# Performance work log

Hardware: AMD Instinct MI355X
Metric: run time of the kernel (lower is better)

## Reference

```python
import jax, jax.numpy as jnp
import numpy as np
from jax import lax

B, CIN, HID, COUT = 64, 256, 256, 10
MULTI, KS = 3, 3
TH = TW = 7      # template (kernel) input spatial size
SH = SW = 31     # search input spatial size
EPS = 1e-5
DN = ('NCHW', 'OIHW', 'NCHW')


def _conv(x, w):
    return lax.conv_general_dilated(x, w, (1, 1), 'VALID', dimension_numbers=DN)


def _bn(x, p):
    # p: [4, C] packed (gamma, beta, running_mean, running_var); inference-mode BN
    g, b, m, v = p[0], p[1], p[2], p[3]
    inv = g / jnp.sqrt(v + EPS)
    return x * inv[:, None, None] + (b - m * inv)[:, None, None]


def _dwxcorr(x, k):
    # per-sample depthwise cross-correlation via groups = B*C trick
    b, c, h, w = x.shape
    kh, kw = k.shape[2], k.shape[3]
    y = lax.conv_general_dilated(
        x.reshape(1, b * c, h, w), k.reshape(b * c, 1, kh, kw),
        (1, 1), 'VALID', dimension_numbers=DN, feature_group_count=b * c)
    return y.reshape(b, c, y.shape[2], y.shape[3])


def _multixcorr(search, kernel):
    # crop template feature to 5x5 / 3x3 / 1x1 sub-kernels, xcorr each,
    # center-crop outputs to the common (smallest) size, concat on channels
    kh = kernel.shape[2]
    feats = []
    for i in range(MULTI):
        kk = kernel[:, :, i:kh - i, i:kh - i]
        o = _dwxcorr(search, kk)
        if i > 0:
            o = o[:, :, i:o.shape[2] - i, i:o.shape[3] - i]
        feats.append(o)
    return jnp.concatenate(feats, axis=1)  # [B, MULTI*HID, 25, 25]


def setup_inputs() -> dict:
    key = jax.random.key(0)
    ks = jax.random.split(key, 12)
    f32 = jnp.float32
    return {
        'kernel': jax.random.normal(ks[0], (B, CIN, TH, TW), f32),
        'search': jax.random.normal(ks[1], (B, CIN, SH, SW), f32),
        'wk': jax.random.normal(ks[2], (HID, CIN, KS, KS), f32) * 0.05,
        'bnk': jax.random.uniform(ks[3], (4, HID), f32, 0.1, 1.0),
        'ws': jax.random.normal(ks[4], (HID, CIN, KS, KS), f32) * 0.05,
        'bns': jax.random.uniform(ks[5], (4, HID), f32, 0.1, 1.0),
        'wd': jax.random.normal(ks[6], (HID, CIN * MULTI, 1, 1), f32) * 0.05,
        'bnd': jax.random.uniform(ks[7], (4, HID), f32, 0.1, 1.0),
        'wh1': jax.random.normal(ks[8], (HID, HID, 1, 1), f32) * 0.05,
        'bnh': jax.random.uniform(ks[9], (4, HID), f32, 0.1, 1.0),
        'wh2': jax.random.normal(ks[10], (COUT, HID, 1, 1), f32) * 0.05,
        'bh2': jax.random.normal(ks[11], (COUT,), f32) * 0.05,
    }


def reference(kernel, search, wk, bnk, ws, bns, wd, bnd, wh1, bnh, wh2, bh2):
    k = jax.nn.relu(_bn(_conv(kernel, wk), bnk))   # [B, HID, 5, 5]
    s = jax.nn.relu(_bn(_conv(search, ws), bns))   # [B, HID, 29, 29]
    feature = _multixcorr(s, k)                    # [B, 3*HID, 25, 25]
    feature = _bn(_conv(feature, wd), bnd)         # [B, HID, 25, 25]
    h = jax.nn.relu(_bn(_conv(feature, wh1), bnh))
    out = _conv(h, wh2) + bh2[:, None, None]       # [B, COUT, 25, 25]
    return out
```

## Files before the change

kernel.cpp:

```cpp
#include <hip/hip_runtime.h>
#include <hip/hip_bf16.h>
#include <cstdint>
#include <cstddef>

#define EPSBN 1e-5f

typedef unsigned short u16;
typedef unsigned int u32;
typedef _Float16 f16;
typedef _Float16 f16x8 __attribute__((ext_vector_type(8)));
typedef float f32x4 __attribute__((ext_vector_type(4)));

__device__ __forceinline__ void async_copy16(void* lds, const void* g) {
    __builtin_amdgcn_global_load_lds(
        (const __attribute__((address_space(1))) u32*)g,
        (__attribute__((address_space(3))) u32*)lds, 16, 0, 0);
}

__global__ __launch_bounds__(256) void prep_all(
    const float* __restrict__ sin, f16* __restrict__ sa,
    const float* __restrict__ kin, f16* __restrict__ ka,
    const float* __restrict__ wk, const float* __restrict__ ws,
    const float* __restrict__ wd, const float* __restrict__ wh1,
    const float* __restrict__ wh2, f16* __restrict__ bpk,
    f16* __restrict__ bps, f16* __restrict__ bpd, f16* __restrict__ bp1,
    f16* __restrict__ bp2) {
    __shared__ float tile[64][65];
    int t = blockIdx.x;
    int tid = threadIdx.x;
    if (t < 4352) {
        int b = t / 68;
        int rem = t - b * 68;
        int c0 = (rem / 17) * 64;
        int z = rem % 17;
        bool isk = (z == 16);
        const float* in = isk ? kin : sin;
        f16* op = isk ? ka : sa;
        int HW = isk ? 49 : 961;
        int h0 = isk ? 0 : z * 64;
        int cl = tid >> 6;
        int hl = tid & 63;
        for (int r = cl; r < 64; r += 4) {
            int hw = h0 + hl;
            tile[r][hl] =
                (hw < HW) ? in[(size_t)(b * 256 + c0 + r) * HW + hw] : 0.f;
        }
        __syncthreads();
        int c = tid & 63;
        for (int r = cl; r < 64; r += 4) {
            int hw = h0 + r;
            if (hw < HW)
                op[((size_t)b * HW + hw) * 256 + c0 + c] = (f16)tile[c][r];
        }
        return;
    }
    int blk = t - 4352;
    const float* W;
    f16* Bp;
    int nK32, OCr, K, i;
    bool conv = false;
    if (blk < 2304) {
        W = wk; Bp = bpk; nK32 = 72; OCr = 256; K = 2304; conv = true;
        i = blk * 256 + tid;
    } else if (blk < 4608) {
        W = ws; Bp = bps; nK32 = 72; OCr = 256; K = 2304; conv = true;
        i = (blk - 2304) * 256 + tid;
    } else if (blk < 5376) {
        W = wd; Bp = bpd; nK32 = 24; OCr = 256; K = 768;
        i = (blk - 4608) * 256 + tid;
    } else if (blk < 5632) {
        W = wh1; Bp = bp1; nK32 = 8; OCr = 256; K = 256;
        i = (blk - 5376) * 256 + tid;
    } else {
        W = wh2; Bp = bp2; nK32 = 8; OCr = 10; K = 256;
        i = (blk - 5632) * 256 + tid;
    }
    int per = nK32 * 512;
    int oct = i / per;
    int r = i - oct * per;
    int k32 = r >> 9;
    int lr = r & 511;
    int l = lr >> 3, j = lr & 7;
    int oc = oct * 16 + (l & 15);
    int k = k32 * 32 + ((l >> 4) << 3) + j;
    float v = 0.f;
    if (oc < OCr)
        v = conv ? W[(size_t)(oc * 256 + (k & 255)) * 9 + (k >> 8)]
                 : W[(size_t)oc * K + k];
    Bp[(size_t)(oct * nK32 + k32) * 512 + lr] = (f16)v;
}

template <int KHW, int EPI>
__device__ __forceinline__ void gemm8_body(
    f16* lds, const f16* __restrict__ A, const f16* __restrict__ Bp,
    const float* __restrict__ bnp, float* __restrict__ outF,
    f16* __restrict__ oF, int m0, int M, int OC, int C, int H, int W,
    int OH, int OW) {
    const int Ktot = KHW * C;
    const int nKt = Ktot >> 6;
    const int nI = nKt >> 1;
    const int nK32 = Ktot >> 5;
    const int tid = threadIdx.x;
    const int lane = tid & 63;
    const int wid = tid >> 6;
    const int rowl = lane & 15;
    const int quad = lane >> 4;
    const int wm = wid >> 2;
    const int wn = wid & 3;
    const int OHW = OH * OW;

    int arow[4];
#pragma unroll
    for (int h = 0; h < 2; ++h)
#pragma unroll
        for (int s = 0; s < 2; ++s) {
            int ml = ((wid & 4) << 5) + h * 64 + (wid & 3) * 16 + s * 8 +
                     (lane >> 3);
            int m = m0 + ml;
            if (m >= M) m = M - 1;
            int b = m / OHW;
            int r = m - b * OHW;
            int y = r / OW;
            int x = r - y * OW;
            arow[h * 2 + s] = ((b * H + y) * W + x) * C +
                              (((lane & 7) ^ (lane >> 3)) << 3);
        }
    int bsrcb[2];
#pragma unroll
    for (int h = 0; h < 2; ++h) {
        int slot = h * 8 + wid;
        int o = ((slot >> 1) & 3) * 4 + ((slot >> 3) << 1) + (slot & 1);
        bsrcb[h] = o * nK32 * 512 + lane * 8;
    }

    auto koff_of = [&](int kt) {
        if (KHW == 9) {
            int pos = kt >> 2;
            int ky = pos / 3, kx = pos - ky * 3;
            return (ky * W + kx) * C + ((kt & 3) << 6);
        }
        return kt << 6;
    };
    auto stageA = [&](int buf, int h, int kt) {
        int koff = koff_of(kt);
#pragma unroll
        for (int s = 0; s < 2; ++s)
            async_copy16(
                &lds[buf * 16384 +
                     ((h * 1024 + wid * 128 + s * 64 + lane) << 3)],
                A + arow[h * 2 + s] + koff);
    };
    auto stageB = [&](int buf, int h, int kt) {
#pragma unroll
        for (int s = 0; s < 2; ++s)
            async_copy16(
                &lds[32768 + buf * 16384 +
                     ((((h * 8 + wid) * 2 + s) * 64 + lane) << 3)],
                Bp + bsrcb[h] + (kt * 2 + s) * 512);
    };

    f32x4 acc[8][4];
#pragma unroll
    for (int i = 0; i < 8; ++i)
#pragma unroll
        for (int j = 0; j < 4; ++j) acc[i][j] = (f32x4)0.f;

    f16x8 ah[4][2], bhA[2][2], bhB[2][2];

    auto dsA = [&](int buf, int qm) {
#pragma unroll
        for (int ii = 0; ii < 4; ++ii) {
            int g = qm * 128 + wm * 64 + ii * 16 + rowl;
#pragma unroll
            for (int ks = 0; ks < 2; ++ks)
                ah[ii][ks] = *(const f16x8*)&lds[
                    buf * 16384 + g * 64 +
                    ((((ks << 2) | quad) ^ (rowl & 7)) << 3)];
        }
    };
    auto dsB = [&](int buf, int qn, f16x8 (&bh)[2][2]) {
#pragma unroll
        for (int jj = 0; jj < 2; ++jj) {
            int slot = qn * 8 + wn * 2 + jj;
#pragma unroll
            for (int ks = 0; ks < 2; ++ks)
                bh[jj][ks] = *(const f16x8*)&lds[
                    32768 + buf * 16384 + (slot * 2 + ks) * 512 + lane * 8];
        }
    };

#define MFMA_QUAD(qm, qn, bh)                                            \
    do {                                                                 \
        _Pragma("unroll") for (int ks = 0; ks < 2; ++ks)                 \
            _Pragma("unroll") for (int ii = 0; ii < 4; ++ii)             \
                _Pragma("unroll") for (int jj = 0; jj < 2; ++jj)         \
                    acc[(qm)*4 + ii][(qn)*2 + jj] =                      \
                        __builtin_amdgcn_mfma_f32_16x16x32_f16(          \
                            ah[ii][ks], bh[jj][ks],                      \
                            acc[(qm)*4 + ii][(qn)*2 + jj], 0, 0, 0);     \
    } while (0)

#define PH_TAIL(MF)                                        \
    __builtin_amdgcn_s_barrier();                          \
    asm volatile("s_waitcnt lgkmcnt(0)" ::: "memory");     \
    __builtin_amdgcn_s_setprio(1);                         \
    MF;                                                    \
    __builtin_amdgcn_s_setprio(0)

    stageA(0, 0, 0);
    stageA(0, 1, 0);
    stageB(0, 0, 0);
    stageB(0, 1, 0);
    stageA(1, 0, 1);
    stageB(1, 0, 1);
    stageB(1, 1, 1);
    asm volatile("s_waitcnt vmcnt(6)" ::: "memory");
    __builtin_amdgcn_s_barrier();

    for (int it = 0; it < nI; ++it) {
        const bool more = (it + 1 < nI);
        const int t2 = 2 * it + 2;
        const int t3 = 2 * it + 3;
        dsA(0, 0);
        dsB(0, 0, bhA);
        stageA(1, 1, 2 * it + 1);
        PH_TAIL(MFMA_QUAD(0, 0, bhA));
        __builtin_amdgcn_s_barrier();
        dsB(0, 1, bhB);
        if (more) stageA(0, 0, t2);
        PH_TAIL(MFMA_QUAD(0, 1, bhB));
        __builtin_amdgcn_s_barrier();
        dsA(0, 1);
        if (more) stageB(0, 0, t2);
        PH_TAIL(MFMA_QUAD(1, 0, bhA));
        __builtin_amdgcn_s_barrier();
        if (more) stageB(0, 1, t2);
        PH_TAIL(MFMA_QUAD(1, 1, bhB));
        if (more)
            asm volatile("s_waitcnt vmcnt(6)" ::: "memory");
        else
            asm volatile("s_waitcnt vmcnt(0)" ::: "memory");
        __builtin_amdgcn_s_barrier();
        dsA(1, 0);
        dsB(1, 0, bhA);
        if (more) stageA(0, 1, t2);
        PH_TAIL(MFMA_QUAD(0, 0, bhA));
        __builtin_amdgcn_s_barrier();
        dsB(1, 1, bhB);
        if (more) stageA(1, 0, t3);
        PH_TAIL(MFMA_QUAD(0, 1, bhB));
        __builtin_amdgcn_s_barrier();
        dsA(1, 1);
        if (more) stageB(1, 0, t3);
        PH_TAIL(MFMA_QUAD(1, 0, bhA));
        __builtin_amdgcn_s_barrier();
        if (more) stageB(1, 1, t3);
        PH_TAIL(MFMA_QUAD(1, 1, bhB));
        if (more) asm volatile("s_waitcnt vmcnt(6)" ::: "memory");
        __builtin_amdgcn_s_barrier();
    }
#undef PH_TAIL
#undef MFMA_QUAD

#pragma unroll
    for (int j = 0; j < 4; ++j) {
        int oc = wn * 64 + j * 16 + rowl;
        bool ocv = oc < OC;
        float scale = 1.f, shift = 0.f;
        if (ocv) {
            if (EPI != 3) {
                float g = bnp[oc];
                float bb = bnp[OC + oc];
                float mm = bnp[2 * OC + oc];
                float vv = bnp[3 * OC + oc];
                float inv = g * rsqrtf(vv + EPSBN);
                scale = inv;
                shift = bb - mm * inv;
            } else {
                shift = bnp[oc];
            }
        }
#pragma unroll
        for (int i = 0; i < 8; ++i) {
#pragma unroll
            for (int r = 0; r < 4; ++r) {
                int m = m0 + wm * 128 + i * 16 + quad * 4 + r;
                if (m < M && ocv) {
                    float v = acc[i][j][r] * scale + shift;
                    if (EPI == 2) v = fmaxf(v, 0.f);
                    if (EPI == 3) {
                        int b = m / OHW;
                        int rr = m - b * OHW;
                        outF[((size_t)b * OC + oc) * OHW + rr] = v;
                    } else {
                        oF[(size_t)m * OC + oc] = (f16)v;
                    }
                }
            }
        }
    }
}

__global__ __launch_bounds__(512, 2) void conv33_fused8(
    const f16* sA_g, const f16* bpS, const float* bns, f16* sOut,
    const f16* kA_g, const f16* bpK, const float* bnk, f16* kOut) {
    __shared__ f16 lds[65536];
    bool sec = blockIdx.x < 7;
    const f16* A = sec ? kA_g : sA_g;
    const f16* Bp = sec ? bpK : bpS;
    const float* bnp = sec ? bnk : bns;
    f16* oF = sec ? kOut : sOut;
    int M = sec ? 1600 : 53824;
    int Hh = sec ? 7 : 31;
    int OHs = sec ? 5 : 29;
    int m0 = (sec ? blockIdx.x : (blockIdx.x - 7)) * 256;
    gemm8_body<9, 2>(lds, A, Bp, bnp, nullptr, oF, m0, M, 256, 256, Hh, Hh,
                     OHs, OHs);
}

__global__ __launch_bounds__(256, 2) void head_fused(
    const f16* __restrict__ feat, const f16* __restrict__ bpd,
    const float* __restrict__ bnd, const f16* __restrict__ bp1,
    const float* __restrict__ bnh, const f16* __restrict__ bp2,
    const float* __restrict__ bh2, float* __restrict__ out) {
    __shared__ f16 lds[40960];
    const int F2B = 20480;
    const int tid = threadIdx.x;
    const int lane = tid & 63;
    const int rowl = lane & 15;
    const int quad = lane >> 4;
    const int wn = tid >> 6;
    const int m0 = blockIdx.x * 80;

    int asrc[5];
#pragma unroll
    for (int s = 0; s < 5; ++s) {
        int idx = tid + s * 256;
        int ml = idx >> 4;
        int qs = (idx & 15) ^ (ml & 15);
        asrc[s] = ml * 768 + qs * 8;
    }
    auto issueA = [&](int buf, int kb) {
#pragma unroll
        for (int s = 0; s < 5; ++s)
            async_copy16(&lds[buf * 10240 + (tid + s * 256) * 8],
                         feat + (size_t)m0 * 768 + asrc[s] + kb * 128);
    };
    auto loadB = [&](f16x8(&bh)[4][4], const f16* __restrict__ Bp, int nK32,
                     int kb) {
#pragma unroll
        for (int ks = 0; ks < 4; ++ks)
#pragma unroll
            for (int j = 0; j < 4; ++j)
                bh[ks][j] = *(const f16x8*)&Bp[((size_t)((wn * 4 + j) * nK32 +
                                                         kb * 4 + ks)) *
                                                   512 +
                                               lane * 8];
    };

    f32x4 acc[5][4];
#pragma unroll
    for (int i = 0; i < 5; ++i)
#pragma unroll
        for (int j = 0; j < 4; ++j) acc[i][j] = (f32x4)0.f;

    auto computeS1 = [&](int buf, f16x8(&bh)[4][4]) {
#pragma unroll
        for (int ks = 0; ks < 4; ++ks) {
            f16x8 ah[5];
#pragma unroll
            for (int i = 0; i < 5; ++i)
                ah[i] = *(const f16x8*)&lds[buf * 10240 +
                                            (i * 16 + rowl) * 128 +
                                            ((((ks << 2) | quad) ^ rowl)
                                             << 3)];
#pragma unroll
            for (int i = 0; i < 5; ++i)
#pragma unroll
                for (int j = 0; j < 4; ++j)
                    acc[i][j] = __builtin_amdgcn_mfma_f32_16x16x32_f16(
                        ah[i], bh[ks][j], acc[i][j], 0, 0, 0);
        }
    };
    auto tileRd = [&](int kb, int ks, int i) {
        int g = i * 16 + rowl;
        int kc = kb * 16 + (ks << 2) + quad;
        int sw = (kc & 24) | ((kc ^ rowl) & 7);
        return *(const f16x8*)&lds[F2B + g * 256 + (sw << 3)];
    };

    f16x8 bh0[4][4], bh1[4][4];
    issueA(0, 0);
    loadB(bh0, bpd, 24, 0);
    for (int kb = 0; kb < 6; kb += 2) {
        __syncthreads();
        issueA(1, kb + 1);
        loadB(bh1, bpd, 24, kb + 1);
        computeS1(0, bh0);
        __syncthreads();
        if (kb + 2 < 6) {
            issueA(0, kb + 2);
            loadB(bh0, bpd, 24, kb + 2);
        }
        computeS1(1, bh1);
    }
#pragma unroll
    for (int j = 0; j < 4; ++j) {
        int oc = wn * 64 + j * 16 + rowl;
        float g = bnd[oc], bb = bnd[256 + oc], mm = bnd[512 + oc],
              vv = bnd[768 + oc];
        float inv = g * rsqrtf(vv + EPSBN);
        float shift = bb - mm * inv;
        int c = oc >> 3;
#pragma unroll
        for (int i = 0; i < 5; ++i)
#pragma unroll
            for (int r = 0; r < 4; ++r) {
                int row = i * 16 + quad * 4 + r;
                int sw = (c & 24) | ((c ^ row) & 7);
                lds[F2B + row * 256 + (sw << 3) + (oc & 7)] =
                    (f16)(acc[i][j][r] * inv + shift);
            }
    }
    loadB(bh0, bp1, 8, 0);
    __syncthreads();

#pragma unroll
    for (int i = 0; i < 5; ++i)
#pragma unroll
        for (int j = 0; j < 4; ++j) acc[i][j] = (f32x4)0.f;
    loadB(bh1, bp1, 8, 1);
#pragma unroll
    for (int kb = 0; kb < 2; ++kb) {
#pragma unroll
        for (int ks = 0; ks < 4; ++ks) {
            f16x8 ah[5];
#pragma unroll
            for (int i = 0; i < 5; ++i) ah[i] = tileRd(kb, ks, i);
#pragma unroll
            for (int i = 0; i < 5; ++i)
#pragma unroll
                for (int j = 0; j < 4; ++j)
                    acc[i][j] = __builtin_amdgcn_mfma_f32_16x16x32_f16(
                        ah[i], kb ? bh1[ks][j] : bh0[ks][j], acc[i][j], 0, 0,
                        0);
        }
    }
    __syncthreads();
#pragma unroll
    for (int j = 0; j < 4; ++j) {
        int oc = wn * 64 + j * 16 + rowl;
        float g = bnh[oc], bb = bnh[256 + oc], mm = bnh[512 + oc],
              vv = bnh[768 + oc];
        float inv = g * rsqrtf(vv + EPSBN);
        float shift = bb - mm * inv;
        int c = oc >> 3;
#pragma unroll
        for (int i = 0; i < 5; ++i)
#pragma unroll
            for (int r = 0; r < 4; ++r) {
                int row = i * 16 + quad * 4 + r;
                int sw = (c & 24) | ((c ^ row) & 7);
                lds[F2B + row * 256 + (sw << 3) + (oc & 7)] =
                    (f16)fmaxf(acc[i][j][r] * inv + shift, 0.f);
            }
    }
    __syncthreads();
    if (wn != 0) return;

    f32x4 a3[5];
#pragma unroll
    for (int i = 0; i < 5; ++i) a3[i] = (f32x4)0.f;
#pragma unroll
    for (int kb = 0; kb < 2; ++kb)
#pragma unroll
        for (int ks = 0; ks < 4; ++ks) {
            f16x8 b3 =
                *(const f16x8*)&bp2[(size_t)(kb * 4 + ks) * 512 + lane * 8];
#pragma unroll
            for (int i = 0; i < 5; ++i)
                a3[i] = __builtin_amdgcn_mfma_f32_16x16x32_f16(
                    tileRd(kb, ks, i), b3, a3[i], 0, 0, 0);
        }
    int oc = rowl;
    if (oc < 10) {
        float shift = bh2[oc];
#pragma unroll
        for (int i = 0; i < 5; ++i)
#pragma unroll
            for (int r = 0; r < 4; ++r) {
                int m = m0 + i * 16 + quad * 4 + r;
                int b = m / 625;
                int rr = m - b * 625;
                out[((size_t)b * 10 + oc) * 625 + rr] = a3[i][r] + shift;
            }
    }
}

__global__ __launch_bounds__(256) void xcorr_nhwc(
    const f16* __restrict__ sf, const f16* __restrict__ kf,
    f16* __restrict__ feat) {
    int by = blockIdx.x;
    int b = by / 25;
    int y = by - b * 25;
    int c = threadIdx.x;
    float kv[25];
#pragma unroll
    for (int p = 0; p < 25; ++p)
        kv[p] = (float)kf[(size_t)(b * 25 + p) * 256 + c];
    const f16* srow = sf + (size_t)(b * 29 + y) * 29 * 256 + c;
    float sv[25];
#pragma unroll
    for (int d = 0; d < 5; ++d)
#pragma unroll
        for (int e = 0; e < 5; ++e)
            sv[d * 5 + e] = (float)srow[(size_t)(d * 29 + e) * 256];
#pragma unroll
    for (int x = 0; x < 25; ++x) {
        float a2 = sv[12] * kv[12];
        float a1 = a2;
#pragma unroll
        for (int d = 1; d < 4; ++d)
#pragma unroll
            for (int e = 1; e < 4; ++e)
                if (d != 2 || e != 2)
                    a1 = fmaf(sv[d * 5 + e], kv[d * 5 + e], a1);
        float a0 = a1;
#pragma unroll
        for (int p = 0; p < 25; ++p) {
            int d = p / 5, e = p % 5;
            if (d == 0 || d == 4 || e == 0 || e == 4)
                a0 = fmaf(sv[p], kv[p], a0);
        }
        size_t o = ((size_t)by * 25 + x) * 768 + c;
        feat[o] = (f16)a0;
        feat[o + 256] = (f16)a1;
        feat[o + 512] = (f16)a2;
        if (x < 24) {
#pragma unroll
            for (int d = 0; d < 5; ++d) {
#pragma unroll
                for (int e = 0; e < 4; ++e) sv[d * 5 + e] = sv[d * 5 + e + 1];
                sv[d * 5 + 4] = (float)srow[(size_t)(d * 29 + x + 5) * 256];
            }
        }
    }
}

extern "C" void kernel_launch(void* const* d_in, const int* in_sizes, int n_in,
                              void* d_out, int out_size, void* d_ws,
                              size_t ws_size, hipStream_t stream) {
    const float* kernel_in = (const float*)d_in[0];
    const float* search_in = (const float*)d_in[1];
    const float* wk = (const float*)d_in[2];
    const float* bnk = (const float*)d_in[3];
    const float* ws = (const float*)d_in[4];
    const float* bns = (const float*)d_in[5];
    const float* wd = (const float*)d_in[6];
    const float* bnd = (const float*)d_in[7];
    const float* wh1 = (const float*)d_in[8];
    const float* bnh = (const float*)d_in[9];
    const float* wh2 = (const float*)d_in[10];
    const float* bh2 = (const float*)d_in[11];
    float* out = (float*)d_out;

    char* base = (char*)d_ws;
    size_t off = 0;
    auto alloc = [&](size_t bytes) {
        off = (off + 511) & ~(size_t)511;
        void* p = base + off;
        off += bytes;
        return p;
    };

    f16* bpd = (f16*)alloc((size_t)16 * 24 * 512 * 2);
    f16* bp1 = (f16*)alloc((size_t)16 * 8 * 512 * 2);
    f16* bp2 = (f16*)alloc((size_t)8 * 8 * 512 * 2);
    f16* kfeat = (f16*)alloc((size_t)1600 * 256 * 2);
    f16* sfeat = (f16*)alloc((size_t)53824 * 256 * 2);
    size_t P1 = (off + 511) & ~(size_t)511;
    f16* bpk = (f16*)alloc((size_t)16 * 72 * 512 * 2);
    f16* bps = (f16*)alloc((size_t)16 * 72 * 512 * 2);
    f16* ka = (f16*)alloc((size_t)64 * 49 * 256 * 2);
    f16* sa = (f16*)alloc((size_t)64 * 961 * 256 * 2);
    f16* feat = (f16*)(base + P1);

    prep_all<<<dim3(10112), 256, 0, stream>>>(search_in, sa, kernel_in, ka,
                                              wk, ws, wd, wh1, wh2, bpk, bps,
                                              bpd, bp1, bp2);
    conv33_fused8<<<dim3(218), 512, 0, stream>>>(sa, bps, bns, sfeat, ka,
                                                 bpk, bnk, kfeat);
    xcorr_nhwc<<<dim3(1600), 256, 0, stream>>>(sfeat, kfeat, feat);
    head_fused<<<dim3(500), 256, 0, stream>>>(feat, bpd, bnd, bp1, bnh, bp2,
                                              bh2, out);
}
```

Measured before the change: 269.2 us.

## Fuse depthwise xcorr into head kernel, computing features directly into LDS

```diff
diff --git a/kernel.cpp b/kernel.cpp
--- a/kernel.cpp
+++ b/kernel.cpp
@@ -8,6 +8,8 @@
 typedef unsigned short u16;
 typedef unsigned int u32;
 typedef _Float16 f16;
+typedef _Float16 f16x2 __attribute__((ext_vector_type(2)));
+typedef _Float16 f16x4 __attribute__((ext_vector_type(4)));
 typedef _Float16 f16x8 __attribute__((ext_vector_type(8)));
 typedef float f32x4 __attribute__((ext_vector_type(4)));
 
@@ -15,6 +17,24 @@
     __builtin_amdgcn_global_load_lds(
         (const __attribute__((address_space(1))) u32*)g,
         (__attribute__((address_space(3))) u32*)lds, 16, 0, 0);
+}
+
+template <int NK32, int OCR, int KK, bool CONV>
+__device__ __forceinline__ void pack_w(const float* __restrict__ W,
+                                       f16* __restrict__ Bp, int i) {
+    const int per = NK32 * 512;
+    int oct = i / per;
+    int r = i - oct * per;
+    int k32 = r >> 9;
+    int lr = r & 511;
+    int l = lr >> 3, j = lr & 7;
+    int oc = oct * 16 + (l & 15);
+    int k = k32 * 32 + ((l >> 4) << 3) + j;
+    float v = 0.f;
+    if (oc < OCR)
+        v = CONV ? W[(size_t)(oc * 256 + (k & 255)) * 9 + (k >> 8)]
+                 : W[(size_t)oc * KK + k];
+    Bp[(size_t)(oct * NK32 + k32) * 512 + lr] = (f16)v;
 }
 
 __global__ __launch_bounds__(256) void prep_all(
@@ -46,48 +66,31 @@
                 (hw < HW) ? in[(size_t)(b * 256 + c0 + r) * HW + hw] : 0.f;
         }
         __syncthreads();
-        int c = tid & 63;
-        for (int r = cl; r < 64; r += 4) {
+        int cg = (tid & 15) * 4;
+        int rw = tid >> 4;
+#pragma unroll
+        for (int it = 0; it < 4; ++it) {
+            int r = rw + it * 16;
             int hw = h0 + r;
-            if (hw < HW)
-                op[((size_t)b * HW + hw) * 256 + c0 + c] = (f16)tile[c][r];
+            if (hw < HW) {
+                f16x4 v = {(f16)tile[cg][r], (f16)tile[cg + 1][r],
+                           (f16)tile[cg + 2][r], (f16)tile[cg + 3][r]};
+                *(f16x4*)&op[((size_t)b * HW + hw) * 256 + c0 + cg] = v;
+            }
         }
         return;
     }
     int blk = t - 4352;
-    const float* W;
-    f16* Bp;
-    int nK32, OCr, K, i;
-    bool conv = false;
-    if (blk < 2304) {
-        W = wk; Bp = bpk; nK32 = 72; OCr = 256; K = 2304; conv = true;
-        i = blk * 256 + tid;
-    } else if (blk < 4608) {
-        W = ws; Bp = bps; nK32 = 72; OCr = 256; K = 2304; conv = true;
-        i = (blk - 2304) * 256 + tid;
-    } else if (blk < 5376) {
-        W = wd; Bp = bpd; nK32 = 24; OCr = 256; K = 768;
-        i = (blk - 4608) * 256 + tid;
-    } else if (blk < 5632) {
-        W = wh1; Bp = bp1; nK32 = 8; OCr = 256; K = 256;
-        i = (blk - 5376) * 256 + tid;
-    } else {
-        W = wh2; Bp = bp2; nK32 = 8; OCr = 10; K = 256;
-        i = (blk - 5632) * 256 + tid;
-    }
-    int per = nK32 * 512;
-    int oct = i / per;
-    int r = i - oct * per;
-    int k32 = r >> 9;
-    int lr = r & 511;
-    int l = lr >> 3, j = lr & 7;
-    int oc = oct * 16 + (l & 15);
-    int k = k32 * 32 + ((l >> 4) << 3) + j;
-    float v = 0.f;
-    if (oc < OCr)
-        v = conv ? W[(size_t)(oc * 256 + (k & 255)) * 9 + (k >> 8)]
-                 : W[(size_t)oc * K + k];
-    Bp[(size_t)(oct * nK32 + k32) * 512 + lr] = (f16)v;
+    if (blk < 2304)
+        pack_w<72, 256, 2304, true>(wk, bpk, blk * 256 + tid);
+    else if (blk < 4608)
+        pack_w<72, 256, 2304, true>(ws, bps, (blk - 2304) * 256 + tid);
+    else if (blk < 5376)
+        pack_w<24, 256, 768, false>(wd, bpd, (blk - 4608) * 256 + tid);
+    else if (blk < 5632)
+        pack_w<8, 256, 256, false>(wh1, bp1, (blk - 5376) * 256 + tid);
+    else
+        pack_w<8, 10, 256, false>(wh2, bp2, (blk - 5632) * 256 + tid);
 }
 
 template <int KHW, int EPI>
@@ -319,10 +322,11 @@
 }
 
 __global__ __launch_bounds__(256, 2) void head_fused(
-    const f16* __restrict__ feat, const f16* __restrict__ bpd,
-    const float* __restrict__ bnd, const f16* __restrict__ bp1,
-    const float* __restrict__ bnh, const f16* __restrict__ bp2,
-    const float* __restrict__ bh2, float* __restrict__ out) {
+    const f16* __restrict__ sf, const f16* __restrict__ kf,
+    const f16* __restrict__ bpd, const float* __restrict__ bnd,
+    const f16* __restrict__ bp1, const float* __restrict__ bnh,
+    const f16* __restrict__ bp2, const float* __restrict__ bh2,
+    float* __restrict__ out) {
     __shared__ f16 lds[40960];
     const int F2B = 20480;
     const int tid = threadIdx.x;
@@ -331,21 +335,10 @@
     const int quad = lane >> 4;
     const int wn = tid >> 6;
     const int m0 = blockIdx.x * 80;
-
-    int asrc[5];
-#pragma unroll
-    for (int s = 0; s < 5; ++s) {
-        int idx = tid + s * 256;
-        int ml = idx >> 4;
-        int qs = (idx & 15) ^ (ml & 15);
-        asrc[s] = ml * 768 + qs * 8;
-    }
-    auto issueA = [&](int buf, int kb) {
-#pragma unroll
-        for (int s = 0; s < 5; ++s)
-            async_copy16(&lds[buf * 10240 + (tid + s * 256) * 8],
-                         feat + (size_t)m0 * 768 + asrc[s] + kb * 128);
-    };
+    const int c = tid;
+    const int cx = c >> 3;
+    const int c7 = c & 7;
+
     auto loadB = [&](f16x8(&bh)[4][4], const f16* __restrict__ Bp, int nK32,
                      int kb) {
 #pragma unroll
@@ -357,6 +350,12 @@
                                                    512 +
                                                lane * 8];
     };
+    auto tileRdAt = [&](int base, int w, int ks, int i) {
+        int g = i * 16 + rowl;
+        int kc = w * 16 + (ks << 2) + quad;
+        int sw = (kc & 24) | ((kc ^ rowl) & 7);
+        return *(const f16x8*)&lds[base + g * 256 + (sw << 3)];
+    };
 
     f32x4 acc[5][4];
 #pragma unroll
@@ -364,16 +363,12 @@
 #pragma unroll
         for (int j = 0; j < 4; ++j) acc[i][j] = (f32x4)0.f;
 
-    auto computeS1 = [&](int buf, f16x8(&bh)[4][4]) {
+    auto computeW = [&](int base, int w, f16x8(&bh)[4][4]) {
 #pragma unroll
         for (int ks = 0; ks < 4; ++ks) {
             f16x8 ah[5];
 #pragma unroll
-            for (int i = 0; i < 5; ++i)
-                ah[i] = *(const f16x8*)&lds[buf * 10240 +
-                                            (i * 16 + rowl) * 128 +
-                                            ((((ks << 2) | quad) ^ rowl)
-                                             << 3)];
+            for (int i = 0; i < 5; ++i) ah[i] = tileRdAt(base, w, ks, i);
 #pragma unroll
             for (int i = 0; i < 5; ++i)
 #pragma unroll
@@ -382,28 +377,102 @@
                         ah[i], bh[ks][j], acc[i][j], 0, 0, 0);
         }
     };
-    auto tileRd = [&](int kb, int ks, int i) {
-        int g = i * 16 + rowl;
-        int kc = kb * 16 + (ks << 2) + quad;
-        int sw = (kc & 24) | ((kc ^ rowl) & 7);
-        return *(const f16x8*)&lds[F2B + g * 256 + (sw << 3)];
-    };
-
+
+    {
+        int row = 0;
+        while (row < 80) {
+            int m = m0 + row;
+            int b = m / 625;
+            int rem = m - b * 625;
+            int y = rem / 25;
+            int x0 = rem - y * 25;
+            int len = 25 - x0;
+            if (len > 80 - row) len = 80 - row;
+            float kv[25];
+#pragma unroll
+            for (int p = 0; p < 25; ++p)
+                kv[p] = (float)kf[(size_t)(b * 25 + p) * 256 + c];
+            const f16* srow =
+                sf + ((size_t)(b * 29 + y) * 29 + x0) * 256 + c;
+            float sv[25];
+#pragma unroll
+            for (int d = 0; d < 5; ++d)
+#pragma unroll
+                for (int e = 0; e < 5; ++e)
+                    sv[d * 5 + e] = (float)srow[(size_t)(d * 29 + e) * 256];
+            for (int xx = 0;; ++xx) {
+                float a1 = 0.f;
+#pragma unroll
+                for (int d = 1; d < 4; ++d)
+#pragma unroll
+                    for (int e = 1; e < 4; ++e)
+                        a1 = fmaf(sv[d * 5 + e], kv[d * 5 + e], a1);
+                float a0 = a1;
+#pragma unroll
+                for (int p = 0; p < 25; ++p) {
+                    int d = p / 5, e = p % 5;
+                    if (d == 0 || d == 4 || e == 0 || e == 4)
+                        a0 = fmaf(sv[p], kv[p], a0);
+                }
+                int r = row + xx;
+                int swz = ((cx & 24) | ((cx ^ r) & 7)) << 3;
+                lds[r * 256 + swz + c7] = (f16)a0;
+                lds[F2B + r * 256 + swz + c7] = (f16)a1;
+                if (xx + 1 >= len) break;
+#pragma unroll
+                for (int d = 0; d < 5; ++d) {
+#pragma unroll
+                    for (int e = 0; e < 4; ++e)
+                        sv[d * 5 + e] = sv[d * 5 + e + 1];
+                    sv[d * 5 + 4] =
+                        (float)srow[(size_t)(d * 29 + xx + 5) * 256];
+                }
+            }
+            row += len;
+        }
+    }
     f16x8 bh0[4][4], bh1[4][4];
-    issueA(0, 0);
     loadB(bh0, bpd, 24, 0);
-    for (int kb = 0; kb < 6; kb += 2) {
-        __syncthreads();
-        issueA(1, kb + 1);
-        loadB(bh1, bpd, 24, kb + 1);
-        computeS1(0, bh0);
-        __syncthreads();
-        if (kb + 2 < 6) {
-            issueA(0, kb + 2);
-            loadB(bh0, bpd, 24, kb + 2);
-        }
-        computeS1(1, bh1);
-    }
+    __syncthreads();
+
+    loadB(bh1, bpd, 24, 1);
+    computeW(0, 0, bh0);
+    loadB(bh0, bpd, 24, 2);
+    computeW(0, 1, bh1);
+    __syncthreads();
+
+    {
+        int row = 0;
+        while (row < 80) {
+            int m = m0 + row;
+            int b = m / 625;
+            int rem = m - b * 625;
+            int y = rem / 25;
+            int x0 = rem - y * 25;
+            int len = 25 - x0;
+            if (len > 80 - row) len = 80 - row;
+            float k12 = (float)kf[(size_t)(b * 25 + 12) * 256 + c];
+            const f16* sp =
+                sf + ((size_t)(b * 29 + y + 2) * 29 + x0 + 2) * 256 + c;
+            for (int xx = 0; xx < len; ++xx) {
+                float a = (float)sp[(size_t)xx * 256] * k12;
+                int r = row + xx;
+                int swz = ((cx & 24) | ((cx ^ r) & 7)) << 3;
+                lds[r * 256 + swz + c7] = (f16)a;
+            }
+            row += len;
+        }
+    }
+    loadB(bh1, bpd, 24, 3);
+    computeW(F2B, 0, bh0);
+    computeW(F2B, 1, bh1);
+    loadB(bh0, bpd, 24, 4);
+    loadB(bh1, bpd, 24, 5);
+    __syncthreads();
+
+    computeW(0, 0, bh0);
+    computeW(0, 1, bh1);
+
 #pragma unroll
     for (int j = 0; j < 4; ++j) {
         int oc = wn * 64 + j * 16 + rowl;
@@ -411,13 +480,13 @@
               vv = bnd[768 + oc];
         float inv = g * rsqrtf(vv + EPSBN);
         float shift = bb - mm * inv;
-        int c = oc >> 3;
+        int cc = oc >> 3;
 #pragma unroll
         for (int i = 0; i < 5; ++i)
 #pragma unroll
             for (int r = 0; r < 4; ++r) {
                 int row = i * 16 + quad * 4 + r;
-                int sw = (c & 24) | ((c ^ row) & 7);
+                int sw = (cc & 24) | ((cc ^ row) & 7);
                 lds[F2B + row * 256 + (sw << 3) + (oc & 7)] =
                     (f16)(acc[i][j][r] * inv + shift);
             }
@@ -430,22 +499,8 @@
 #pragma unroll
         for (int j = 0; j < 4; ++j) acc[i][j] = (f32x4)0.f;
     loadB(bh1, bp1, 8, 1);
-#pragma unroll
-    for (int kb = 0; kb < 2; ++kb) {
-#pragma unroll
-        for (int ks = 0; ks < 4; ++ks) {
-            f16x8 ah[5];
-#pragma unroll
-            for (int i = 0; i < 5; ++i) ah[i] = tileRd(kb, ks, i);
-#pragma unroll
-            for (int i = 0; i < 5; ++i)
-#pragma unroll
-                for (int j = 0; j < 4; ++j)
-                    acc[i][j] = __builtin_amdgcn_mfma_f32_16x16x32_f16(
-                        ah[i], kb ? bh1[ks][j] : bh0[ks][j], acc[i][j], 0, 0,
-                        0);
-        }
-    }
+    computeW(F2B, 0, bh0);
+    computeW(F2B, 1, bh1);
     __syncthreads();
 #pragma unroll
     for (int j = 0; j < 4; ++j) {
@@ -454,13 +509,13 @@
               vv = bnh[768 + oc];
         float inv = g * rsqrtf(vv + EPSBN);
         float shift = bb - mm * inv;
-        int c = oc >> 3;
+        int cc = oc >> 3;
 #pragma unroll
         for (int i = 0; i < 5; ++i)
 #pragma unroll
             for (int r = 0; r < 4; ++r) {
                 int row = i * 16 + quad * 4 + r;
-                int sw = (c & 24) | ((c ^ row) & 7);
+                int sw = (cc & 24) | ((cc ^ row) & 7);
                 lds[F2B + row * 256 + (sw << 3) + (oc & 7)] =
                     (f16)fmaxf(acc[i][j][r] * inv + shift, 0.f);
             }
@@ -480,7 +535,7 @@
 #pragma unroll
             for (int i = 0; i < 5; ++i)
                 a3[i] = __builtin_amdgcn_mfma_f32_16x16x32_f16(
-                    tileRd(kb, ks, i), b3, a3[i], 0, 0, 0);
+                    tileRdAt(F2B, kb, ks, i), b3, a3[i], 0, 0, 0);
         }
     int oc = rowl;
     if (oc < 10) {
@@ -494,56 +549,6 @@
                 int rr = m - b * 625;
                 out[((size_t)b * 10 + oc) * 625 + rr] = a3[i][r] + shift;
             }
-    }
-}
-
-__global__ __launch_bounds__(256) void xcorr_nhwc(
-    const f16* __restrict__ sf, const f16* __restrict__ kf,
-    f16* __restrict__ feat) {
-    int by = blockIdx.x;
-    int b = by / 25;
-    int y = by - b * 25;
-    int c = threadIdx.x;
-    float kv[25];
-#pragma unroll
-    for (int p = 0; p < 25; ++p)
-        kv[p] = (float)kf[(size_t)(b * 25 + p) * 256 + c];
-    const f16* srow = sf + (size_t)(b * 29 + y) * 29 * 256 + c;
-    float sv[25];
-#pragma unroll
-    for (int d = 0; d < 5; ++d)
-#pragma unroll
-        for (int e = 0; e < 5; ++e)
-            sv[d * 5 + e] = (float)srow[(size_t)(d * 29 + e) * 256];
-#pragma unroll
-    for (int x = 0; x < 25; ++x) {
-        float a2 = sv[12] * kv[12];
-        float a1 = a2;
-#pragma unroll
-        for (int d = 1; d < 4; ++d)
-#pragma unroll
-            for (int e = 1; e < 4; ++e)
-                if (d != 2 || e != 2)
-                    a1 = fmaf(sv[d * 5 + e], kv[d * 5 + e], a1);
-        float a0 = a1;
-#pragma unroll
-        for (int p = 0; p < 25; ++p) {
-            int d = p / 5, e = p % 5;
-            if (d == 0 || d == 4 || e == 0 || e == 4)
-                a0 = fmaf(sv[p], kv[p], a0);
-        }
-        size_t o = ((size_t)by * 25 + x) * 768 + c;
-        feat[o] = (f16)a0;
-        feat[o + 256] = (f16)a1;
-        feat[o + 512] = (f16)a2;
-        if (x < 24) {
-#pragma unroll
-            for (int d = 0; d < 5; ++d) {
-#pragma unroll
-                for (int e = 0; e < 4; ++e) sv[d * 5 + e] = sv[d * 5 + e + 1];
-                sv[d * 5 + 4] = (float)srow[(size_t)(d * 29 + x + 5) * 256];
-            }
-        }
     }
 }
 
@@ -578,19 +583,16 @@
     f16* bp2 = (f16*)alloc((size_t)8 * 8 * 512 * 2);
     f16* kfeat = (f16*)alloc((size_t)1600 * 256 * 2);
     f16* sfeat = (f16*)alloc((size_t)53824 * 256 * 2);
-    size_t P1 = (off + 511) & ~(size_t)511;
     f16* bpk = (f16*)alloc((size_t)16 * 72 * 512 * 2);
     f16* bps = (f16*)alloc((size_t)16 * 72 * 512 * 2);
     f16* ka = (f16*)alloc((size_t)64 * 49 * 256 * 2);
     f16* sa = (f16*)alloc((size_t)64 * 961 * 256 * 2);
-    f16* feat = (f16*)(base + P1);
 
     prep_all<<<dim3(10112), 256, 0, stream>>>(search_in, sa, kernel_in, ka,
                                               wk, ws, wd, wh1, wh2, bpk, bps,
                                               bpd, bp1, bp2);
     conv33_fused8<<<dim3(218), 512, 0, stream>>>(sa, bps, bns, sfeat, ka,
                                                  bpk, bnk, kfeat);
-    xcorr_nhwc<<<dim3(1600), 256, 0, stream>>>(sfeat, kfeat, feat);
-    head_fused<<<dim3(500), 256, 0, stream>>>(feat, bpd, bnd, bp1, bnh, bp2,
-                                              bh2, out);
-}
+    head_fused<<<dim3(500), 256, 0, stream>>>(sfeat, kfeat, bpd, bnd, bp1,
+                                              bnh, bp2, bh2, out);
+}
```

Measured after the change: 295.5 us. 9.8% more time.
